# Kernel tuning notes

Measured on AMD Instinct MI355X. Metric: run time of the kernel, lower is better.

The kernel has to match this reference:

```python
import jax, jax.numpy as jnp
import numpy as np

FRACTION_BITS = 16
INTEGER_BITS = 16


def round_to_fixed(x):
    # floor-quantize to 2^-16 steps, clamp to signed 16-bit integer range
    delta = 2.0 ** (-FRACTION_BITS)
    bound = 2.0 ** (INTEGER_BITS - 1)
    return jnp.clip(jnp.floor(x / delta) * delta, -bound, bound - 1.0)


def setup_inputs() -> dict:
    key = jax.random.key(0)
    k1, k2, k3, k4 = jax.random.split(key, 4)
    N, IN_F, OUT_F = 4096, 4096, 4096
    inp = jax.random.normal(k1, (N, IN_F), dtype=jnp.float32)
    # reset_parameters: shift ~ U(-10,-1), sign ~ U(-1,0), bias ~ U(-b,b), b=1/sqrt(fan_in)
    shift = jax.random.uniform(k2, (OUT_F, IN_F), minval=-10.0, maxval=-1.0, dtype=jnp.float32)
    sign = jax.random.uniform(k3, (OUT_F, IN_F), minval=-1.0, maxval=0.0, dtype=jnp.float32)
    b = 1.0 / np.sqrt(IN_F)
    bias = jax.random.uniform(k4, (OUT_F,), minval=-b, maxval=b, dtype=jnp.float32)
    return {"input": inp, "shift": shift, "sign": sign, "bias": bias}


def reference(input, shift, sign, bias):
    # eager (non-kernel) path of LinearShiftFunction.forward
    q_in = round_to_fixed(input)
    q_bias = round_to_fixed(bias)
    s = jnp.clip(sign, -1.0, 1.0)
    v = jnp.exp2(jnp.round(shift)) * jnp.sign(s)  # [out_f, in_f] power-of-two weights
    out = q_in @ v.T + q_bias[None, :]
    return out
```

## Files before the change

### kernel.cpp

```cpp
#include <hip/hip_runtime.h>
#include <hip/hip_bf16.h>


#define BM 256
#define BN 256
#define BK 64

typedef __bf16 bf16_t;
typedef __attribute__((ext_vector_type(8))) __bf16 bf16x8;
typedef __attribute__((ext_vector_type(4))) __bf16 bf16x4;
typedef __attribute__((ext_vector_type(4))) float f32x4;

__device__ __forceinline__ float q16(float x) {
    float f = floorf(x * 65536.0f) * (1.0f / 65536.0f);
    return fminf(fmaxf(f, -32768.0f), 32767.0f);
}

__global__ void quant_input_kernel(const float* __restrict__ in,
                                   bf16_t* __restrict__ out, int nvec) {
    int stride = gridDim.x * blockDim.x;
    for (int i = blockIdx.x * blockDim.x + threadIdx.x; i < nvec; i += stride) {
        float4 v = reinterpret_cast<const float4*>(in)[i];
        bf16x4 o;
        o[0] = (bf16_t)q16(v.x);
        o[1] = (bf16_t)q16(v.y);
        o[2] = (bf16_t)q16(v.z);
        o[3] = (bf16_t)q16(v.w);
        reinterpret_cast<bf16x4*>(out)[i] = o;
    }
}

__global__ void make_weight_kernel(const float* __restrict__ shift,
                                   const float* __restrict__ sign_,
                                   bf16_t* __restrict__ out, int nvec) {
    int stride = gridDim.x * blockDim.x;
    for (int i = blockIdx.x * blockDim.x + threadIdx.x; i < nvec; i += stride) {
        float4 sh = reinterpret_cast<const float4*>(shift)[i];
        float4 sg = reinterpret_cast<const float4*>(sign_)[i];
        float shs[4] = {sh.x, sh.y, sh.z, sh.w};
        float sgs[4] = {sg.x, sg.y, sg.z, sg.w};
        bf16x4 o;
#pragma unroll
        for (int j = 0; j < 4; ++j) {
            float s = fminf(fmaxf(sgs[j], -1.0f), 1.0f);
            float sv = (s > 0.0f) ? 1.0f : ((s < 0.0f) ? -1.0f : 0.0f);
            o[j] = (bf16_t)(exp2f(rintf(shs[j])) * sv);
        }
        reinterpret_cast<bf16x4*>(out)[i] = o;
    }
}


#define VMW(N) asm volatile("s_waitcnt vmcnt(" #N ")" ::: "memory")
#define LGKM(N) asm volatile("s_waitcnt lgkmcnt(" #N ")" ::: "memory")
#define SBAR0() __builtin_amdgcn_sched_barrier(0)
#define BARF() do { __builtin_amdgcn_s_barrier(); asm volatile("" ::: "memory"); } while (0)

#define STAGE(LDSOFF, SRC) do {                                                          \
    const bf16_t* _s = (SRC);                                                            \
    bf16_t* _d = &lds[(LDSOFF)] + tid * 8;                                               \
    __builtin_amdgcn_global_load_lds((const __attribute__((address_space(1))) void*)_s,  \
                                     (__attribute__((address_space(3))) void*)_d,        \
                                     16, 0, 0);                                          \
    __builtin_amdgcn_global_load_lds(                                                    \
        (const __attribute__((address_space(1))) void*)(_s + (size_t)64 * K),            \
        (__attribute__((address_space(3))) void*)(_d + 4096), 16, 0, 0);                 \
} while (0)

#define READ_A(BUF, MH) do {                                                             \
    const bf16_t* _As = &lds[(BUF) * 32768 + wm * 8192];                                 \
    _Pragma("unroll") for (int m = 0; m < 4; ++m)                                        \
        _Pragma("unroll") for (int kk = 0; kk < 2; ++kk)                                 \
            af[m][kk] = *(const bf16x8*)&_As[((MH) * 64 + m * 16 + fr) * 64 +            \
                                             ((((kk << 2) | hi) ^ fr7) << 3)];           \
} while (0)

#define READ_B(BUF, NH, BF) do {                                                         \
    const bf16_t* _Bs = &lds[(BUF) * 32768 + 16384 + (wn >> 1) * 8192];                  \
    _Pragma("unroll") for (int n = 0; n < 2; ++n)                                        \
        _Pragma("unroll") for (int kk = 0; kk < 2; ++kk)                                 \
            BF[n][kk] = *(const bf16x8*)&_Bs[((wn & 1) * 64 + ((NH) * 2 + n) * 16 + fr)  \
                                                 * 64 +                                  \
                                             ((((kk << 2) | hi) ^ fr7) << 3)];           \
} while (0)

#define QUAD(MH, NH, BF) do {                                                            \
    _Pragma("unroll") for (int m = 0; m < 4; ++m)                                        \
        _Pragma("unroll") for (int n = 0; n < 2; ++n)                                    \
            _Pragma("unroll") for (int kk = 0; kk < 2; ++kk)                             \
                acc[(MH) * 4 + m][(NH) * 2 + n] =                                        \
                    __builtin_amdgcn_mfma_f32_16x16x32_bf16(                             \
                        af[m][kk], BF[n][kk], acc[(MH) * 4 + m][(NH) * 2 + n], 0, 0, 0); \
} while (0)

#define MFMA_PH(MH, NH, BF)                                                              \
    __builtin_amdgcn_s_setprio(1);                                                       \
    QUAD(MH, NH, BF);                                                                    \
    __builtin_amdgcn_s_setprio(0);

#define TILE(BUF, T, S01, S23, ENDW) do {                                                \
                                                                            \
    READ_A(BUF, 0);                                                                      \
    READ_B(BUF, 0, b0f);                                                                 \
    if (S01) STAGE(((BUF) ^ 1) * 32768 + 3 * 8192, srcB1 + (size_t)((T) + 1) * 64);      \
    LGKM(0); SBAR0();                                                                    \
    MFMA_PH(0, 0, b0f)                                                                   \
                                                                            \
    READ_B(BUF, 1, b1f);                                                                 \
    if (S01) STAGE(((BUF) ^ 1) * 32768 + 1 * 8192, srcA1 + (size_t)((T) + 1) * 64);      \
    LGKM(0); SBAR0();                                                                    \
    MFMA_PH(0, 1, b1f)                                                                   \
    BARF();                                                      \
                                                                            \
    READ_A(BUF, 1);                                                                      \
    if (S23) STAGE((BUF) * 32768 + 2 * 8192, srcB0 + (size_t)((T) + 2) * 64);            \
    LGKM(0); SBAR0();                                                                    \
    MFMA_PH(1, 0, b0f)                                                                   \
                                          \
    if (S23) STAGE((BUF) * 32768 + 0 * 8192, srcA0 + (size_t)((T) + 2) * 64);            \
    SBAR0();                                                                             \
    MFMA_PH(1, 1, b1f)                                                                   \
    if ((ENDW) == 4) VMW(4);                                                             \
    else if ((ENDW) == 0) VMW(0);                                                        \
    BARF();                                                           \
} while (0)

__global__ __launch_bounds__(512, 2)
void gemm256_kernel(const bf16_t* __restrict__ A,
                    const bf16_t* __restrict__ B,
                    const float* __restrict__ bias,
                    float* __restrict__ C,
                    int M, int N, int K) {
    __shared__ bf16_t lds[65536];

    const int ntn = N / BN;
    const int nwg = gridDim.x;
    const int q = nwg >> 3, r = nwg & 7;
    const int xcd = blockIdx.x & 7, lid = blockIdx.x >> 3;
    const int swz = (xcd < r ? xcd * (q + 1) : r * (q + 1) + (xcd - r) * q) + lid;
    const int tile_m = (swz / ntn) * BM;
    const int tile_n = (swz % ntn) * BN;

    const int tid = threadIdx.x;
    const int lane = tid & 63;
    const int wid = tid >> 6;
    const int wm = wid >> 2;
    const int wn = wid & 3;
    const int fr = lane & 15;
    const int hi = lane >> 4;
    const int fr7 = fr & 7;

    const int colsrc_e = ((((tid & 7) * 16) ^ ((tid & 56) << 1)) >> 1);
    const bf16_t* srcA0 = A + (size_t)(tile_m + (tid >> 3)) * K + colsrc_e;
    const bf16_t* srcA1 = srcA0 + (size_t)128 * K;
    const bf16_t* srcB0 = B + (size_t)(tile_n + (tid >> 3)) * K + colsrc_e;
    const bf16_t* srcB1 = srcB0 + (size_t)128 * K;

    bf16x8 af[4][2], b0f[2][2], b1f[2][2];
    f32x4 acc[8][4] = {};

    STAGE(16384, srcB0);
    STAGE(0, srcA0);
    STAGE(24576, srcB1);
    STAGE(8192, srcA1);
    STAGE(32768 + 16384, srcB0 + 64);
    STAGE(32768 + 0, srcA0 + 64);
    VMW(4);
    BARF();

    const int npairs = K / 128;
    for (int i = 0; i < npairs - 1; ++i) {
        TILE(0, 2 * i, 1, 1, 4);
        TILE(1, 2 * i + 1, 1, 1, 4);
    }
    TILE(0, 2 * npairs - 2, 1, 0, 0);
    TILE(1, 2 * npairs - 1, 0, 0, -1);

    float qb[4];
#pragma unroll
    for (int ng = 0; ng < 4; ++ng)
        qb[ng] = q16(bias[tile_n + wn * 64 + ng * 16 + fr]);
#pragma unroll
    for (int mg = 0; mg < 8; ++mg) {
        const int grow0 = tile_m + wm * 128 + mg * 16 + hi * 4;
#pragma unroll
        for (int ng = 0; ng < 4; ++ng) {
            const int gcol = tile_n + wn * 64 + ng * 16 + fr;
#pragma unroll
            for (int rr = 0; rr < 4; ++rr)
                C[(size_t)(grow0 + rr) * N + gcol] = acc[mg][ng][rr] + qb[ng];
        }
    }
}

extern "C" void kernel_launch(void* const* d_in, const int* in_sizes, int n_in,
                              void* d_out, int out_size, void* d_ws, size_t ws_size,
                              hipStream_t stream) {
    const float* inp   = (const float*)d_in[0];
    const float* shift = (const float*)d_in[1];
    const float* sign_ = (const float*)d_in[2];
    const float* bias  = (const float*)d_in[3];
    float* out = (float*)d_out;

    const int OUT_F = in_sizes[3];
    const int IN_F  = in_sizes[1] / OUT_F;
    const int Mrows = in_sizes[0] / IN_F;

    bf16_t* Aq = (bf16_t*)d_ws;
    bf16_t* Wq = Aq + (size_t)Mrows * IN_F;

    const int nA = Mrows * IN_F;
    const int nW = OUT_F * IN_F;

    quant_input_kernel<<<2048, 256, 0, stream>>>(inp, Aq, nA >> 2);
    make_weight_kernel<<<2048, 256, 0, stream>>>(shift, sign_, Wq, nW >> 2);

    dim3 grid((Mrows / BM) * (OUT_F / BN));
    gemm256_kernel<<<grid, 512, 0, stream>>>(Aq, Wq, bias, out,
                                             Mrows, OUT_F, IN_F);
}
```

Before: 159.2 us.

## Switch GEMM to 32x32x16 MFMA with K-split LDS layout

Replaces the 16x16x32 bf16 MFMA tiling with 32x32x16 instructions. Each wave now holds a 4x2 grid of 32x32 accumulators, and the LDS staging is reorganized into four 32-wide K slices with a new XOR swizzle and a row stride of 128 between the two loads. The intent is fewer MFMA issues and fewer LDS fragment reads per unit of work, since the larger instruction reuses each fragment more. The epilogue is remapped to the 32x32 output layout. The new swizzle risks LDS bank conflicts, and the epilogue stores may coalesce differently.

Result: slower. 182.5 us (+14.6%).

```diff
diff --git a/kernel.cpp b/kernel.cpp
--- a/kernel.cpp
+++ b/kernel.cpp
@@ -9,7 +9,7 @@
 typedef __bf16 bf16_t;
 typedef __attribute__((ext_vector_type(8))) __bf16 bf16x8;
 typedef __attribute__((ext_vector_type(4))) __bf16 bf16x4;
-typedef __attribute__((ext_vector_type(4))) float f32x4;
+typedef __attribute__((ext_vector_type(16))) float f32x16;
 
 __device__ __forceinline__ float q16(float x) {
     float f = floorf(x * 65536.0f) * (1.0f / 65536.0f);
@@ -63,63 +63,51 @@
                                      (__attribute__((address_space(3))) void*)_d,        \
                                      16, 0, 0);                                          \
     __builtin_amdgcn_global_load_lds(                                                    \
-        (const __attribute__((address_space(1))) void*)(_s + (size_t)64 * K),            \
+        (const __attribute__((address_space(1))) void*)(_s + (size_t)128 * K),           \
         (__attribute__((address_space(3))) void*)(_d + 4096), 16, 0, 0);                 \
 } while (0)
 
-#define READ_A(BUF, MH) do {                                                             \
-    const bf16_t* _As = &lds[(BUF) * 32768 + wm * 8192];                                 \
+#define READ_AB(BUF, KS) do {                                                            \
+    const bf16_t* _As = &lds[(BUF) * 32768 + ((KS) >> 1) * 8192];                        \
+    const bf16_t* _Bs = &lds[(BUF) * 32768 + 16384 + ((KS) >> 1) * 8192];                \
+    const int _p = (((((KS) & 1) << 1) | hi2) ^ l3) * 8;                                 \
     _Pragma("unroll") for (int m = 0; m < 4; ++m)                                        \
-        _Pragma("unroll") for (int kk = 0; kk < 2; ++kk)                                 \
-            af[m][kk] = *(const bf16x8*)&_As[((MH) * 64 + m * 16 + fr) * 64 +            \
-                                             ((((kk << 2) | hi) ^ fr7) << 3)];           \
-} while (0)
-
-#define READ_B(BUF, NH, BF) do {                                                         \
-    const bf16_t* _Bs = &lds[(BUF) * 32768 + 16384 + (wn >> 1) * 8192];                  \
+        af[m] = *(const bf16x8*)&_As[(wm * 128 + m * 32 + l31) * 32 + _p];               \
     _Pragma("unroll") for (int n = 0; n < 2; ++n)                                        \
-        _Pragma("unroll") for (int kk = 0; kk < 2; ++kk)                                 \
-            BF[n][kk] = *(const bf16x8*)&_Bs[((wn & 1) * 64 + ((NH) * 2 + n) * 16 + fr)  \
-                                                 * 64 +                                  \
-                                             ((((kk << 2) | hi) ^ fr7) << 3)];           \
-} while (0)
-
-#define QUAD(MH, NH, BF) do {                                                            \
+        bf[n] = *(const bf16x8*)&_Bs[(wn * 64 + n * 32 + l31) * 32 + _p];                \
+} while (0)
+
+#define MFMA8() do {                                                                     \
+    __builtin_amdgcn_s_setprio(1);                                                       \
     _Pragma("unroll") for (int m = 0; m < 4; ++m)                                        \
         _Pragma("unroll") for (int n = 0; n < 2; ++n)                                    \
-            _Pragma("unroll") for (int kk = 0; kk < 2; ++kk)                             \
-                acc[(MH) * 4 + m][(NH) * 2 + n] =                                        \
-                    __builtin_amdgcn_mfma_f32_16x16x32_bf16(                             \
-                        af[m][kk], BF[n][kk], acc[(MH) * 4 + m][(NH) * 2 + n], 0, 0, 0); \
-} while (0)
-
-#define MFMA_PH(MH, NH, BF)                                                              \
-    __builtin_amdgcn_s_setprio(1);                                                       \
-    QUAD(MH, NH, BF);                                                                    \
-    __builtin_amdgcn_s_setprio(0);
+            acc[m][n] = __builtin_amdgcn_mfma_f32_32x32x16_bf16(                         \
+                af[m], bf[n], acc[m][n], 0, 0, 0);                                       \
+    __builtin_amdgcn_s_setprio(0);                                                       \
+} while (0)
 
 #define TILE(BUF, T, S01, S23, ENDW) do {                                                \
-                                                                            \
-    READ_A(BUF, 0);                                                                      \
-    READ_B(BUF, 0, b0f);                                                                 \
-    if (S01) STAGE(((BUF) ^ 1) * 32768 + 3 * 8192, srcB1 + (size_t)((T) + 1) * 64);      \
-    LGKM(0); SBAR0();                                                                    \
-    MFMA_PH(0, 0, b0f)                                                                   \
-                                                                            \
-    READ_B(BUF, 1, b1f);                                                                 \
-    if (S01) STAGE(((BUF) ^ 1) * 32768 + 1 * 8192, srcA1 + (size_t)((T) + 1) * 64);      \
-    LGKM(0); SBAR0();                                                                    \
-    MFMA_PH(0, 1, b1f)                                                                   \
-    BARF();                                                      \
-                                                                            \
-    READ_A(BUF, 1);                                                                      \
-    if (S23) STAGE((BUF) * 32768 + 2 * 8192, srcB0 + (size_t)((T) + 2) * 64);            \
-    LGKM(0); SBAR0();                                                                    \
-    MFMA_PH(1, 0, b0f)                                                                   \
-                                          \
-    if (S23) STAGE((BUF) * 32768 + 0 * 8192, srcA0 + (size_t)((T) + 2) * 64);            \
-    SBAR0();                                                                             \
-    MFMA_PH(1, 1, b1f)                                                                   \
+                                                                      \
+    READ_AB(BUF, 0);                                                                     \
+    if (S01) STAGE(((BUF) ^ 1) * 32768 + 24576, srcB + (size_t)((T) + 1) * 64 + 32);     \
+    LGKM(0); SBAR0();                                                                    \
+    MFMA8();                                                                             \
+                                                                      \
+    READ_AB(BUF, 1);                                                                     \
+    if (S01) STAGE(((BUF) ^ 1) * 32768 + 8192, srcA + (size_t)((T) + 1) * 64 + 32);      \
+    LGKM(0); SBAR0();                                                                    \
+    MFMA8();                                                                             \
+    BARF();             \
+                                                                      \
+    READ_AB(BUF, 2);                                                                     \
+    if (S23) STAGE((BUF) * 32768 + 16384, srcB + (size_t)((T) + 2) * 64);                \
+    LGKM(0); SBAR0();                                                                    \
+    MFMA8();                                                                             \
+                                                                      \
+    READ_AB(BUF, 3);                                                                     \
+    if (S23) STAGE((BUF) * 32768 + 0, srcA + (size_t)((T) + 2) * 64);                    \
+    LGKM(0); SBAR0();                                                                    \
+    MFMA8();                                                                             \
     if ((ENDW) == 4) VMW(4);                                                             \
     else if ((ENDW) == 0) VMW(0);                                                        \
     BARF();                                                           \
@@ -146,25 +134,23 @@
     const int wid = tid >> 6;
     const int wm = wid >> 2;
     const int wn = wid & 3;
-    const int fr = lane & 15;
-    const int hi = lane >> 4;
-    const int fr7 = fr & 7;
-
-    const int colsrc_e = ((((tid & 7) * 16) ^ ((tid & 56) << 1)) >> 1);
-    const bf16_t* srcA0 = A + (size_t)(tile_m + (tid >> 3)) * K + colsrc_e;
-    const bf16_t* srcA1 = srcA0 + (size_t)128 * K;
-    const bf16_t* srcB0 = B + (size_t)(tile_n + (tid >> 3)) * K + colsrc_e;
-    const bf16_t* srcB1 = srcB0 + (size_t)128 * K;
-
-    bf16x8 af[4][2], b0f[2][2], b1f[2][2];
-    f32x4 acc[8][4] = {};
-
-    STAGE(16384, srcB0);
-    STAGE(0, srcA0);
-    STAGE(24576, srcB1);
-    STAGE(8192, srcA1);
-    STAGE(32768 + 16384, srcB0 + 64);
-    STAGE(32768 + 0, srcA0 + 64);
+    const int l31 = lane & 31;
+    const int hi2 = lane >> 5;
+    const int l3 = lane & 3;
+
+    const int koff = (((tid & 3) ^ ((tid >> 2) & 3)) << 3);
+    const bf16_t* srcA = A + (size_t)(tile_m + (tid >> 2)) * K + koff;
+    const bf16_t* srcB = B + (size_t)(tile_n + (tid >> 2)) * K + koff;
+
+    bf16x8 af[4], bf[2];
+    f32x16 acc[4][2] = {};
+
+    STAGE(0, srcA);
+    STAGE(16384, srcB);
+    STAGE(8192, srcA + 32);
+    STAGE(24576, srcB + 32);
+    STAGE(32768 + 16384, srcB + 64);
+    STAGE(32768 + 0, srcA + 64);
     VMW(4);
     BARF();
 
@@ -176,19 +162,21 @@
     TILE(0, 2 * npairs - 2, 1, 0, 0);
     TILE(1, 2 * npairs - 1, 0, 0, -1);
 
-    float qb[4];
-#pragma unroll
-    for (int ng = 0; ng < 4; ++ng)
-        qb[ng] = q16(bias[tile_n + wn * 64 + ng * 16 + fr]);
-#pragma unroll
-    for (int mg = 0; mg < 8; ++mg) {
-        const int grow0 = tile_m + wm * 128 + mg * 16 + hi * 4;
-#pragma unroll
-        for (int ng = 0; ng < 4; ++ng) {
-            const int gcol = tile_n + wn * 64 + ng * 16 + fr;
-#pragma unroll
-            for (int rr = 0; rr < 4; ++rr)
-                C[(size_t)(grow0 + rr) * N + gcol] = acc[mg][ng][rr] + qb[ng];
+    float qb[2];
+#pragma unroll
+    for (int n = 0; n < 2; ++n)
+        qb[n] = q16(bias[tile_n + wn * 64 + n * 32 + l31]);
+#pragma unroll
+    for (int m = 0; m < 4; ++m) {
+#pragma unroll
+        for (int n = 0; n < 2; ++n) {
+            const int gcol = tile_n + wn * 64 + n * 32 + l31;
+#pragma unroll
+            for (int reg = 0; reg < 16; ++reg) {
+                const int grow = tile_m + wm * 128 + m * 32 +
+                                 (reg & 3) + 8 * (reg >> 2) + 4 * hi2;
+                C[(size_t)grow * N + gcol] = acc[m][n][reg] + qb[n];
+            }
         }
     }
 }
```
